# Performance work log

Measured on AMD Instinct MI355X. Metric: run time of the kernel, lower is better.

The kernel has to match this reference:

```python
import jax, jax.numpy as jnp
import numpy as np

GAMMA = 0.001

N_TEST, N_TRAIN, D, OUT = 8192, 8192, 512, 16

def setup_inputs() -> dict:
    key = jax.random.key(0)
    k1, k2, k3 = jax.random.split(key, 3)
    X = jax.random.normal(k1, (N_TEST, D), dtype=jnp.float32)
    train_X = jax.random.normal(k2, (N_TRAIN, D), dtype=jnp.float32)
    alpha = jax.random.normal(k3, (N_TRAIN, OUT), dtype=jnp.float32)
    return {"X": X, "train_X": train_X, "alpha": alpha}


def reference(X, train_X, alpha):
    # (same math as (x[:,None]-y[None])**2 summed over d, without the n*m*d blowup)
    x_sq = jnp.sum(X * X, axis=-1, keepdims=True)            # [n_test, 1]
    y_sq = jnp.sum(train_X * train_X, axis=-1)[None, :]       # [1, n_train]
    cross = X @ train_X.T                                     # [n_test, n_train]
    sq = x_sq + y_sq - 2.0 * cross
    K_test = jnp.exp(-GAMMA * sq)
    return K_test @ alpha                                     # [n_test, out]
```

## Files before the change

kernel.cpp:

```cpp
#include <hip/hip_runtime.h>
#include <stdint.h>

#define NROW 8192
#define DIM  512
#define NOUT 16
#define GAMMA 0.001f
#define EXP2S (2.0f * GAMMA * 1.44269504088896340736f)
#define SC1 0x7F7F7F7F

typedef __bf16 bf16_t;
typedef bf16_t bf16x4_t __attribute__((ext_vector_type(4)));
typedef bf16_t bf16x8_t __attribute__((ext_vector_type(8)));
typedef float  floatx4_t __attribute__((ext_vector_type(4)));
typedef int    intx4_t  __attribute__((ext_vector_type(4)));
typedef int    intx8_t  __attribute__((ext_vector_type(8)));

__device__ __forceinline__ void async_copy16(const void* g, const void* l) {
    __builtin_amdgcn_global_load_lds(
        (__attribute__((address_space(1))) void*)(uintptr_t)g,
        (__attribute__((address_space(3))) void*)(uint32_t)(uintptr_t)l,
        16, 0, 0);
}

__global__ __launch_bounds__(256) void prep_convert(
    const float* __restrict__ X, const float* __restrict__ T,
    const float* __restrict__ alpha,
    uint8_t* __restrict__ Xf, uint8_t* __restrict__ Tf,
    float* __restrict__ xfac, bf16_t* __restrict__ alphaTp)
{
    const int w = threadIdx.x >> 6, lane = threadIdx.x & 63;
    const int row = blockIdx.x * 4 + w;
    const bool is_test = row < NROW;
    const float* src = is_test ? X : T;
    uint8_t* dst = is_test ? Xf : Tf;
    const int r = is_test ? row : row - NROW;
    const float4* s4 = (const float4*)(src + (size_t)r * DIM);
    const float4 v0 = s4[lane * 2];
    const float4 v1 = s4[lane * 2 + 1];
    float ss = v0.x*v0.x + v0.y*v0.y + v0.z*v0.z + v0.w*v0.w
             + v1.x*v1.x + v1.y*v1.y + v1.z*v1.z + v1.w*v1.w;
    int lo = __builtin_amdgcn_cvt_pk_fp8_f32(v0.x, v0.y, 0, false);
    lo     = __builtin_amdgcn_cvt_pk_fp8_f32(v0.z, v0.w, lo, true);
    int hi = __builtin_amdgcn_cvt_pk_fp8_f32(v1.x, v1.y, 0, false);
    hi     = __builtin_amdgcn_cvt_pk_fp8_f32(v1.z, v1.w, hi, true);
    *(int2*)(dst + (size_t)r * DIM + lane * 8) = make_int2(lo, hi);
#pragma unroll
    for (int m = 32; m > 0; m >>= 1) ss += __shfl_xor(ss, m, 64);
    const float f = __expf(-GAMMA * ss);
    if (is_test) {
        if (lane == 0) xfac[r] = f;
    } else if (lane < 16) {
        alphaTp[(size_t)lane * NROW + r] = (bf16_t)(alpha[r * 16 + lane] * f);
    }
}

#define TPT 4
#define KLD2 72

__global__ __launch_bounds__(256, 2) void rbf_main(
    const uint8_t* __restrict__ Xf, const uint8_t* __restrict__ Tf,
    const bf16_t* __restrict__ alphaTp, const float* __restrict__ xfac,
    float* __restrict__ out)
{
    __shared__ __align__(16) unsigned char smem[65536];

    const int tid = threadIdx.x;
    const int w = tid >> 6, lane = tid & 63;
    const int wm = w >> 1, wn = w & 1;
    const int quad = lane >> 4, l15 = lane & 15;

    const int rb = blockIdx.x;
    const int chunk = blockIdx.y;
    const int row0 = rb * 128;
    const int cb0 = chunk * (TPT * 128);

    const int s_row = tid >> 3;
    const int s_ub = (((tid & 7) ^ (s_row & 7)) * 16);
    const uint8_t* gXp = Xf + (size_t)(row0 + s_row) * DIM + s_ub;
    const uint8_t* gTp = Tf + (size_t)(cb0 + s_row) * DIM + s_ub;
    const unsigned ldsW = (unsigned)(w << 10);

    const int sw = l15 & 7;

    const floatx4_t vzero = {0.f, 0.f, 0.f, 0.f};
    floatx4_t oacc[4];
#pragma unroll
    for (int i = 0; i < 4; ++i) oacc[i] = vzero;

    bf16_t* kw = (bf16_t*)smem + w * (64 * KLD2);

    for (int t = 0; t < TPT; ++t) {
        const int cb = cb0 + t * 128;
        const uint8_t* gTt = gTp + (size_t)t * 128 * DIM;

        floatx4_t acc[4][4];
#pragma unroll
        for (int i = 0; i < 4; ++i)
#pragma unroll
            for (int j = 0; j < 4; ++j) acc[i][j] = vzero;

        __syncthreads();
#pragma unroll
        for (int i = 0; i < 4; ++i) {
            async_copy16(gTt + (size_t)i * 16384, smem + i * 4096 + ldsW);
            async_copy16(gXp + (size_t)i * 16384, smem + 16384 + i * 4096 + ldsW);
        }

#pragma unroll
        for (int g = 0; g < 4; ++g) {
            __syncthreads();
            if (g < 3) {
                const unsigned bb = ((g + 1) & 1) * 32768u;
                const int kb = (g + 1) * 128;
#pragma unroll
                for (int i = 0; i < 4; ++i) {
                    async_copy16(gTt + (size_t)i * 16384 + kb, smem + bb + i * 4096 + ldsW);
                    async_copy16(gXp + (size_t)i * 16384 + kb, smem + bb + 16384 + i * 4096 + ldsW);
                }
            }
            const unsigned char* bufc = smem + (g & 1) * 32768;
            intx8_t ta[4], xb[4];
#pragma unroll
            for (int i = 0; i < 4; ++i) {
                const int rA = wm * 64 + i * 16 + l15;
                const intx4_t alo = *(const intx4_t*)(bufc + rA * 128 + (((2 * quad) ^ sw) * 16));
                const intx4_t ahi = *(const intx4_t*)(bufc + rA * 128 + (((2 * quad + 1) ^ sw) * 16));
                ta[i] = __builtin_shufflevector(alo, ahi, 0, 1, 2, 3, 4, 5, 6, 7);
                const int rB = wn * 64 + i * 16 + l15;
                const intx4_t blo = *(const intx4_t*)(bufc + 16384 + rB * 128 + (((2 * quad) ^ sw) * 16));
                const intx4_t bhi = *(const intx4_t*)(bufc + 16384 + rB * 128 + (((2 * quad + 1) ^ sw) * 16));
                xb[i] = __builtin_shufflevector(blo, bhi, 0, 1, 2, 3, 4, 5, 6, 7);
            }
#pragma unroll
            for (int mi = 0; mi < 4; ++mi)
#pragma unroll
                for (int ni = 0; ni < 4; ++ni)
                    acc[mi][ni] = __builtin_amdgcn_mfma_scale_f32_16x16x128_f8f6f4(
                        ta[mi], xb[ni], acc[mi][ni], 0, 0, 0, SC1, 0, SC1);
        }

        __syncthreads();
#pragma unroll
        for (int ni = 0; ni < 4; ++ni)
#pragma unroll
            for (int mi = 0; mi < 4; ++mi) {
                bf16x4_t pk;
#pragma unroll
                for (int r = 0; r < 4; ++r)
                    pk[r] = (bf16_t)__builtin_amdgcn_exp2f(acc[mi][ni][r] * EXP2S);
                *(bf16x4_t*)(kw + (ni * 16 + l15) * KLD2 + mi * 16 + quad * 4) = pk;
            }

#pragma unroll
        for (int ks = 0; ks < 2; ++ks) {
            const bf16x8_t bv = *(const bf16x8_t*)(alphaTp + (size_t)l15 * NROW
                                                   + cb + wm * 64 + ks * 32 + quad * 8);
#pragma unroll
            for (int ni = 0; ni < 4; ++ni) {
                const bf16x8_t av = *(const bf16x8_t*)(kw + (ni * 16 + l15) * KLD2
                                                       + ks * 32 + quad * 8);
                oacc[ni] = __builtin_amdgcn_mfma_f32_16x16x32_bf16(av, bv, oacc[ni], 0, 0, 0);
            }
        }
    }

    __syncthreads();
    float* stash = (float*)smem;
    if (wm == 1) {
#pragma unroll
        for (int ni = 0; ni < 4; ++ni)
            *(floatx4_t*)(stash + wn * 1024 + ni * 256 + lane * 4) = oacc[ni];
    }
    __syncthreads();
    if (wm == 0) {
#pragma unroll
        for (int ni = 0; ni < 4; ++ni) {
            const floatx4_t o2 = *(const floatx4_t*)(stash + wn * 1024 + ni * 256 + lane * 4);
            const int trow = row0 + wn * 64 + ni * 16 + quad * 4;
            const float4 xf = *(const float4*)(xfac + trow);
            atomicAdd(out + (size_t)(trow + 0) * NOUT + l15, (oacc[ni][0] + o2[0]) * xf.x);
            atomicAdd(out + (size_t)(trow + 1) * NOUT + l15, (oacc[ni][1] + o2[1]) * xf.y);
            atomicAdd(out + (size_t)(trow + 2) * NOUT + l15, (oacc[ni][2] + o2[2]) * xf.z);
            atomicAdd(out + (size_t)(trow + 3) * NOUT + l15, (oacc[ni][3] + o2[3]) * xf.w);
        }
    }
}

extern "C" void kernel_launch(void* const* d_in, const int* in_sizes, int n_in,
                              void* d_out, int out_size, void* d_ws, size_t ws_size,
                              hipStream_t stream) {
    (void)in_sizes; (void)n_in; (void)out_size; (void)ws_size;
    const float* X     = (const float*)d_in[0];
    const float* T     = (const float*)d_in[1];
    const float* alpha = (const float*)d_in[2];

    char* ws = (char*)d_ws;
    uint8_t* Xf     = (uint8_t*)ws;
    uint8_t* Tf     = (uint8_t*)(ws + (8u << 20));
    float*   xfac   = (float*)(ws + (16u << 20));
    bf16_t*  alphaTp= (bf16_t*)(ws + (16u << 20) + (64u << 10));
    float*   out    = (float*)d_out;

    hipMemsetAsync(out, 0, (size_t)NROW * NOUT * sizeof(float), stream);
    prep_convert<<<4096, 256, 0, stream>>>(X, T, alpha, Xf, Tf, xfac, alphaTp);
    dim3 grid(64, 16);
    rbf_main<<<grid, 256, 0, stream>>>(Xf, Tf, alphaTp, xfac, out);
}
```

Measured before the change: 121.3 us.

## Keep X fragments resident in registers across train tiles, halve LDS

The X (test) tile for each block is now loaded once into registers (4x4 intx8 fragments, 128 VGPRs) before the train-tile loop, instead of being reloaded from global into LDS for every one of the four train tiles. The LDS allocation shrinks from 64KB to the size of the K staging buffer, and only train-tile data is double-buffered. This cuts redundant global and LDS traffic for X and lowers LDS use. The cost is much higher register pressure under launch_bounds(256,2), which risks spills or reduced occupancy.

```diff
diff --git a/kernel.cpp b/kernel.cpp
--- a/kernel.cpp
+++ b/kernel.cpp
@@ -62,7 +62,7 @@
     const bf16_t* __restrict__ alphaTp, const float* __restrict__ xfac,
     float* __restrict__ out)
 {
-    __shared__ __align__(16) unsigned char smem[65536];
+    __shared__ __align__(16) unsigned char smem[4 * 64 * KLD2 * 2];
 
     const int tid = threadIdx.x;
     const int w = tid >> 6, lane = tid & 63;
@@ -81,6 +81,32 @@
     const unsigned ldsW = (unsigned)(w << 10);
 
     const int sw = l15 & 7;
+    const int ub0 = ((2 * quad) ^ sw) * 16;
+    const int ub1 = ((2 * quad + 1) ^ sw) * 16;
+
+    intx8_t xr[4][4];
+#pragma unroll
+    for (int i = 0; i < 4; ++i)
+        async_copy16(gXp + (size_t)i * 16384, smem + i * 4096 + ldsW);
+#pragma unroll
+    for (int g = 0; g < 4; ++g) {
+        __syncthreads();
+        if (g < 3) {
+            const unsigned bb = ((g + 1) & 1) * 16384u;
+#pragma unroll
+            for (int i = 0; i < 4; ++i)
+                async_copy16(gXp + (size_t)i * 16384 + (g + 1) * 128,
+                             smem + bb + i * 4096 + ldsW);
+        }
+        const unsigned char* bufc = smem + (g & 1) * 16384;
+#pragma unroll
+        for (int ni = 0; ni < 4; ++ni) {
+            const int rB = wn * 64 + ni * 16 + l15;
+            const intx4_t blo = *(const intx4_t*)(bufc + rB * 128 + ub0);
+            const intx4_t bhi = *(const intx4_t*)(bufc + rB * 128 + ub1);
+            xr[g][ni] = __builtin_shufflevector(blo, bhi, 0, 1, 2, 3, 4, 5, 6, 7);
+        }
+    }
 
     const floatx4_t vzero = {0.f, 0.f, 0.f, 0.f};
     floatx4_t oacc[4];
@@ -101,42 +127,32 @@
 
         __syncthreads();
 #pragma unroll
-        for (int i = 0; i < 4; ++i) {
+        for (int i = 0; i < 4; ++i)
             async_copy16(gTt + (size_t)i * 16384, smem + i * 4096 + ldsW);
-            async_copy16(gXp + (size_t)i * 16384, smem + 16384 + i * 4096 + ldsW);
-        }
 
 #pragma unroll
         for (int g = 0; g < 4; ++g) {
             __syncthreads();
             if (g < 3) {
-                const unsigned bb = ((g + 1) & 1) * 32768u;
+                const unsigned bb = ((g + 1) & 1) * 16384u;
                 const int kb = (g + 1) * 128;
 #pragma unroll
-                for (int i = 0; i < 4; ++i) {
-                    async_copy16(gTt + (size_t)i * 16384 + kb, smem + bb + i * 4096 + ldsW);
-                    async_copy16(gXp + (size_t)i * 16384 + kb, smem + bb + 16384 + i * 4096 + ldsW);
-                }
-            }
-            const unsigned char* bufc = smem + (g & 1) * 32768;
-            intx8_t ta[4], xb[4];
-#pragma unroll
-            for (int i = 0; i < 4; ++i) {
-                const int rA = wm * 64 + i * 16 + l15;
-                const intx4_t alo = *(const intx4_t*)(bufc + rA * 128 + (((2 * quad) ^ sw) * 16));
-                const intx4_t ahi = *(const intx4_t*)(bufc + rA * 128 + (((2 * quad + 1) ^ sw) * 16));
-                ta[i] = __builtin_shufflevector(alo, ahi, 0, 1, 2, 3, 4, 5, 6, 7);
-                const int rB = wn * 64 + i * 16 + l15;
-                const intx4_t blo = *(const intx4_t*)(bufc + 16384 + rB * 128 + (((2 * quad) ^ sw) * 16));
-                const intx4_t bhi = *(const intx4_t*)(bufc + 16384 + rB * 128 + (((2 * quad + 1) ^ sw) * 16));
-                xb[i] = __builtin_shufflevector(blo, bhi, 0, 1, 2, 3, 4, 5, 6, 7);
-            }
-#pragma unroll
-            for (int mi = 0; mi < 4; ++mi)
+                for (int i = 0; i < 4; ++i)
+                    async_copy16(gTt + (size_t)i * 16384 + kb,
+                                 smem + bb + i * 4096 + ldsW);
+            }
+            const unsigned char* bufc = smem + (g & 1) * 16384;
+#pragma unroll
+            for (int mi = 0; mi < 4; ++mi) {
+                const int rA = wm * 64 + mi * 16 + l15;
+                const intx4_t alo = *(const intx4_t*)(bufc + rA * 128 + ub0);
+                const intx4_t ahi = *(const intx4_t*)(bufc + rA * 128 + ub1);
+                const intx8_t ta = __builtin_shufflevector(alo, ahi, 0, 1, 2, 3, 4, 5, 6, 7);
 #pragma unroll
                 for (int ni = 0; ni < 4; ++ni)
                     acc[mi][ni] = __builtin_amdgcn_mfma_scale_f32_16x16x128_f8f6f4(
-                        ta[mi], xb[ni], acc[mi][ni], 0, 0, 0, SC1, 0, SC1);
+                        ta, xr[g][ni], acc[mi][ni], 0, 0, 0, SC1, 0, SC1);
+            }
         }
 
         __syncthreads();
```

New measurement: 133.2 us. 1.1x slower.

## Pre-pack FP8 operands into MFMA fragment layout and load directly to registers

Applied to the files above, without the earlier changes.

The prep kernel now writes X and train_X in a tiled layout that matches the 32x32x64 FP8 MFMA fragment order. The main kernel drops the LDS double-buffered async staging and its barriers, and each wave loads its fragments from global memory into registers with a one-step register prefetch. It also switches from 16x16x128 to 32x32x64 scaled MFMAs. This removes LDS traffic and syncs, but each wave now fetches its own operands from global/L2 with no sharing through LDS, so latency hiding rests on the shallow prefetch and on occupancy.

```diff
diff --git a/kernel.cpp b/kernel.cpp
--- a/kernel.cpp
+++ b/kernel.cpp
@@ -11,28 +11,28 @@
 typedef __bf16 bf16_t;
 typedef bf16_t bf16x4_t __attribute__((ext_vector_type(4)));
 typedef bf16_t bf16x8_t __attribute__((ext_vector_type(8)));
-typedef float  floatx4_t __attribute__((ext_vector_type(4)));
+typedef float  floatx4_t  __attribute__((ext_vector_type(4)));
+typedef float  floatx16_t __attribute__((ext_vector_type(16)));
 typedef int    intx4_t  __attribute__((ext_vector_type(4)));
 typedef int    intx8_t  __attribute__((ext_vector_type(8)));
 
-__device__ __forceinline__ void async_copy16(const void* g, const void* l) {
-    __builtin_amdgcn_global_load_lds(
-        (__attribute__((address_space(1))) void*)(uintptr_t)g,
-        (__attribute__((address_space(3))) void*)(uint32_t)(uintptr_t)l,
-        16, 0, 0);
+__device__ __forceinline__ intx8_t ld_frag(const uint8_t* p) {
+    const intx4_t lo = *(const intx4_t*)(p);
+    const intx4_t hi = *(const intx4_t*)(p + 16);
+    return __builtin_shufflevector(lo, hi, 0, 1, 2, 3, 4, 5, 6, 7);
 }
 
 __global__ __launch_bounds__(256) void prep_convert(
     const float* __restrict__ X, const float* __restrict__ T,
     const float* __restrict__ alpha,
-    uint8_t* __restrict__ Xf, uint8_t* __restrict__ Tf,
+    uint8_t* __restrict__ X2, uint8_t* __restrict__ T2,
     float* __restrict__ xfac, bf16_t* __restrict__ alphaTp)
 {
     const int w = threadIdx.x >> 6, lane = threadIdx.x & 63;
     const int row = blockIdx.x * 4 + w;
     const bool is_test = row < NROW;
     const float* src = is_test ? X : T;
-    uint8_t* dst = is_test ? Xf : Tf;
+    uint8_t* dst = is_test ? X2 : T2;
     const int r = is_test ? row : row - NROW;
     const float4* s4 = (const float4*)(src + (size_t)r * DIM);
     const float4 v0 = s4[lane * 2];
@@ -43,7 +43,10 @@
     lo     = __builtin_amdgcn_cvt_pk_fp8_f32(v0.z, v0.w, lo, true);
     int hi = __builtin_amdgcn_cvt_pk_fp8_f32(v1.x, v1.y, 0, false);
     hi     = __builtin_amdgcn_cvt_pk_fp8_f32(v1.z, v1.w, hi, true);
-    *(int2*)(dst + (size_t)r * DIM + lane * 8) = make_int2(lo, hi);
+    const int k0 = lane * 8;
+    const size_t off = ((size_t)((r >> 5) * 8 + (k0 >> 6)) << 11)
+                     + (size_t)(((((k0 >> 5) & 1) << 5) | (r & 31)) * 32 + (k0 & 31));
+    *(int2*)(dst + off) = make_int2(lo, hi);
 #pragma unroll
     for (int m = 32; m > 0; m >>= 1) ss += __shfl_xor(ss, m, 64);
     const float f = __expf(-GAMMA * ss);
@@ -58,29 +61,25 @@
 #define KLD2 72
 
 __global__ __launch_bounds__(256, 2) void rbf_main(
-    const uint8_t* __restrict__ Xf, const uint8_t* __restrict__ Tf,
+    const uint8_t* __restrict__ X2, const uint8_t* __restrict__ T2,
     const bf16_t* __restrict__ alphaTp, const float* __restrict__ xfac,
     float* __restrict__ out)
 {
-    __shared__ __align__(16) unsigned char smem[65536];
+    __shared__ __align__(16) unsigned char smem[4 * 64 * KLD2 * 2];
 
     const int tid = threadIdx.x;
     const int w = tid >> 6, lane = tid & 63;
     const int wm = w >> 1, wn = w & 1;
     const int quad = lane >> 4, l15 = lane & 15;
+    const int l31 = lane & 31, lk = lane >> 5;
 
     const int rb = blockIdx.x;
     const int chunk = blockIdx.y;
     const int row0 = rb * 128;
     const int cb0 = chunk * (TPT * 128);
 
-    const int s_row = tid >> 3;
-    const int s_ub = (((tid & 7) ^ (s_row & 7)) * 16);
-    const uint8_t* gXp = Xf + (size_t)(row0 + s_row) * DIM + s_ub;
-    const uint8_t* gTp = Tf + (size_t)(cb0 + s_row) * DIM + s_ub;
-    const unsigned ldsW = (unsigned)(w << 10);
-
-    const int sw = l15 & 7;
+    const uint8_t* xp0 = X2 + (((size_t)(rb * 4 + wn * 2) * 8) << 11) + lane * 32;
+    const uint8_t* xp1 = xp0 + (8 << 11);
 
     const floatx4_t vzero = {0.f, 0.f, 0.f, 0.f};
     floatx4_t oacc[4];
@@ -91,75 +90,63 @@
 
     for (int t = 0; t < TPT; ++t) {
         const int cb = cb0 + t * 128;
-        const uint8_t* gTt = gTp + (size_t)t * 128 * DIM;
+        const uint8_t* tp0 = T2 + (((size_t)(chunk * 16 + t * 4 + wm * 2) * 8) << 11)
+                             + lane * 32;
+        const uint8_t* tp1 = tp0 + (8 << 11);
 
-        floatx4_t acc[4][4];
+        floatx16_t acc[2][2];
 #pragma unroll
-        for (int i = 0; i < 4; ++i)
+        for (int i = 0; i < 2; ++i)
 #pragma unroll
-            for (int j = 0; j < 4; ++j) acc[i][j] = vzero;
+            for (int j = 0; j < 2; ++j)
+#pragma unroll
+                for (int e = 0; e < 16; ++e) acc[i][j][e] = 0.f;
 
-        __syncthreads();
+        intx8_t ca0 = ld_frag(tp0), ca1 = ld_frag(tp1);
+        intx8_t cb0v = ld_frag(xp0), cb1v = ld_frag(xp1);
 #pragma unroll
-        for (int i = 0; i < 4; ++i) {
-            async_copy16(gTt + (size_t)i * 16384, smem + i * 4096 + ldsW);
-            async_copy16(gXp + (size_t)i * 16384, smem + 16384 + i * 4096 + ldsW);
+        for (int s = 0; s < 8; ++s) {
+            intx8_t na0, na1, nb0, nb1;
+            if (s < 7) {
+                na0 = ld_frag(tp0 + (s + 1) * 2048);
+                na1 = ld_frag(tp1 + (s + 1) * 2048);
+                nb0 = ld_frag(xp0 + (s + 1) * 2048);
+                nb1 = ld_frag(xp1 + (s + 1) * 2048);
+            }
+            acc[0][0] = __builtin_amdgcn_mfma_scale_f32_32x32x64_f8f6f4(
+                ca0, cb0v, acc[0][0], 0, 0, 0, SC1, 0, SC1);
+            acc[0][1] = __builtin_amdgcn_mfma_scale_f32_32x32x64_f8f6f4(
+                ca0, cb1v, acc[0][1], 0, 0, 0, SC1, 0, SC1);
+            acc[1][0] = __builtin_amdgcn_mfma_scale_f32_32x32x64_f8f6f4(
+                ca1, cb0v, acc[1][0], 0, 0, 0, SC1, 0, SC1);
+            acc[1][1] = __builtin_amdgcn_mfma_scale_f32_32x32x64_f8f6f4(
+                ca1, cb1v, acc[1][1], 0, 0, 0, SC1, 0, SC1);
+            if (s < 7) { ca0 = na0; ca1 = na1; cb0v = nb0; cb1v = nb1; }
         }
 
 #pragma unroll
-        for (int g = 0; g < 4; ++g) {
-            __syncthreads();
-            if (g < 3) {
-                const unsigned bb = ((g + 1) & 1) * 32768u;
-                const int kb = (g + 1) * 128;
+        for (int ni = 0; ni < 2; ++ni)
 #pragma unroll
-                for (int i = 0; i < 4; ++i) {
-                    async_copy16(gTt + (size_t)i * 16384 + kb, smem + bb + i * 4096 + ldsW);
-                    async_copy16(gXp + (size_t)i * 16384 + kb, smem + bb + 16384 + i * 4096 + ldsW);
+            for (int mi = 0; mi < 2; ++mi)
+#pragma unroll
+                for (int rg = 0; rg < 4; ++rg) {
+                    bf16x4_t pk;
+#pragma unroll
+                    for (int j = 0; j < 4; ++j)
+                        pk[j] = (bf16_t)__builtin_amdgcn_exp2f(acc[mi][ni][rg * 4 + j] * EXP2S);
+                    *(bf16x4_t*)(kw + (ni * 32 + l31) * KLD2
+                                 + mi * 32 + rg * 8 + lk * 4) = pk;
                 }
-            }
-            const unsigned char* bufc = smem + (g & 1) * 32768;
-            intx8_t ta[4], xb[4];
-#pragma unroll
-            for (int i = 0; i < 4; ++i) {
-                const int rA = wm * 64 + i * 16 + l15;
-                const intx4_t alo = *(const intx4_t*)(bufc + rA * 128 + (((2 * quad) ^ sw) * 16));
-                const intx4_t ahi = *(const intx4_t*)(bufc + rA * 128 + (((2 * quad + 1) ^ sw) * 16));
-                ta[i] = __builtin_shufflevector(alo, ahi, 0, 1, 2, 3, 4, 5, 6, 7);
-                const int rB = wn * 64 + i * 16 + l15;
-                const intx4_t blo = *(const intx4_t*)(bufc + 16384 + rB * 128 + (((2 * quad) ^ sw) * 16));
-                const intx4_t bhi = *(const intx4_t*)(bufc + 16384 + rB * 128 + (((2 * quad + 1) ^ sw) * 16));
-                xb[i] = __builtin_shufflevector(blo, bhi, 0, 1, 2, 3, 4, 5, 6, 7);
-            }
-#pragma unroll
-            for (int mi = 0; mi < 4; ++mi)
-#pragma unroll
-                for (int ni = 0; ni < 4; ++ni)
-                    acc[mi][ni] = __builtin_amdgcn_mfma_scale_f32_16x16x128_f8f6f4(
-                        ta[mi], xb[ni], acc[mi][ni], 0, 0, 0, SC1, 0, SC1);
-        }
-
-        __syncthreads();
-#pragma unroll
-        for (int ni = 0; ni < 4; ++ni)
-#pragma unroll
-            for (int mi = 0; mi < 4; ++mi) {
-                bf16x4_t pk;
-#pragma unroll
-                for (int r = 0; r < 4; ++r)
-                    pk[r] = (bf16_t)__builtin_amdgcn_exp2f(acc[mi][ni][r] * EXP2S);
-                *(bf16x4_t*)(kw + (ni * 16 + l15) * KLD2 + mi * 16 + quad * 4) = pk;
-            }
 
 #pragma unroll
         for (int ks = 0; ks < 2; ++ks) {
             const bf16x8_t bv = *(const bf16x8_t*)(alphaTp + (size_t)l15 * NROW
                                                    + cb + wm * 64 + ks * 32 + quad * 8);
 #pragma unroll
-            for (int ni = 0; ni < 4; ++ni) {
-                const bf16x8_t av = *(const bf16x8_t*)(kw + (ni * 16 + l15) * KLD2
+            for (int n4 = 0; n4 < 4; ++n4) {
+                const bf16x8_t av = *(const bf16x8_t*)(kw + (n4 * 16 + l15) * KLD2
                                                        + ks * 32 + quad * 8);
-                oacc[ni] = __builtin_amdgcn_mfma_f32_16x16x32_bf16(av, bv, oacc[ni], 0, 0, 0);
+                oacc[n4] = __builtin_amdgcn_mfma_f32_16x16x32_bf16(av, bv, oacc[n4], 0, 0, 0);
             }
         }
     }
@@ -195,14 +182,14 @@
     const float* alpha = (const float*)d_in[2];
 
     char* ws = (char*)d_ws;
-    uint8_t* Xf     = (uint8_t*)ws;
-    uint8_t* Tf     = (uint8_t*)(ws + (8u << 20));
+    uint8_t* X2     = (uint8_t*)ws;
+    uint8_t* T2     = (uint8_t*)(ws + (8u << 20));
     float*   xfac   = (float*)(ws + (16u << 20));
     bf16_t*  alphaTp= (bf16_t*)(ws + (16u << 20) + (64u << 10));
     float*   out    = (float*)d_out;
 
     hipMemsetAsync(out, 0, (size_t)NROW * NOUT * sizeof(float), stream);
-    prep_convert<<<4096, 256, 0, stream>>>(X, T, alpha, Xf, Tf, xfac, alphaTp);
+    prep_convert<<<4096, 256, 0, stream>>>(X, T, alpha, X2, T2, xfac, alphaTp);
     dim3 grid(64, 16);
-    rbf_main<<<grid, 256, 0, stream>>>(Xf, Tf, alphaTp, xfac, out);
+    rbf_main<<<grid, 256, 0, stream>>>(X2, T2, alphaTp, xfac, out);
 }
```

Result: slower. 133.7 us (+10.2%).
